# Performance work log

Measured on AMD Instinct MI355X. Metric: run time of the kernel, lower is better.

The kernel has to match this reference:

```python
import jax, jax.numpy as jnp
import numpy as np

WS = 8            # window size
OWIN = 12         # overlapping window: int(8*0.5)+8
HEADS = 4
DHEAD = 16
INNER = 64        # HEADS*DHEAD
DIM = 48
B, H, W = 4, 192, 192
HN, WN = H // WS, W // WS
NW = HN * WN
NK = NW // 2      # deterministic hard-token keep count (ratio=0.5, E[gumbel rate]=0.5)
SCALE = DHEAD ** -0.5


def conv1x1(x, w, b=None):
    y = jnp.einsum('bchw,oc->bohw', x, w)
    return y if b is None else y + b[:, None, None]


def win_part(x):
    # 'b c (h dh) (w dw) -> b (h w) (dh dw) c'
    b, c, h, w = x.shape
    x = x.reshape(b, c, h // WS, WS, w // WS, WS).transpose(0, 2, 4, 3, 5, 1)
    return x.reshape(b, (h // WS) * (w // WS), WS * WS, c)


def win_unpart(x, h, w):
    b, n, l, c = x.shape
    x = x.reshape(b, h // WS, w // WS, WS, WS, c).transpose(0, 5, 1, 3, 2, 4)
    return x.reshape(b, c, h, w)


def unfold_overlap(x):
    # nn.Unfold(kernel=OWIN, stride=WS, pad=(OWIN-WS)//2) -> (b, NW, OWIN^2, c)
    pad = (OWIN - WS) // 2
    xp = jnp.pad(x, ((0, 0), (0, 0), (pad, pad), (pad, pad)))
    hi = (jnp.arange(HN) * WS)[:, None] + jnp.arange(OWIN)[None]
    wi = (jnp.arange(WN) * WS)[:, None] + jnp.arange(OWIN)[None]
    p = xp[:, :, hi[:, None, :, None], wi[None, :, None, :]]  # (b,c,HN,WN,OWIN,OWIN)
    b, c = x.shape[:2]
    return p.reshape(b, c, NW, OWIN * OWIN).transpose(0, 2, 3, 1)


def rel_to_abs(x):
    b, l, m = x.shape
    r = (m + 1) // 2
    x = jnp.pad(x, ((0, 0), (0, 0), (0, 1)))
    flat = jnp.pad(x.reshape(b, l * (m + 1)), ((0, 0), (0, m - l)))
    return flat.reshape(b, l + 1, m)[:, :l, m - r:]


def relative_logits_1d(q, rel_k):
    b, h, w, d = q.shape
    r = (rel_k.shape[0] + 1) // 2
    logits = jnp.einsum('bxyd,rd->bxyr', q, rel_k)
    logits = rel_to_abs(logits.reshape(b * h, w, -1)).reshape(b, h, w, r)
    return jnp.broadcast_to(logits[:, :, None, :, :], (b, h, r, w, r))


def rel_pos_emb(q, rel_h, rel_w):
    # q: (B_, WS*WS, d) -> (B_, WS*WS, OWIN*OWIN)
    B_, L, d = q.shape
    q4 = q.reshape(B_, WS, WS, d)
    lw = relative_logits_1d(q4, rel_w).transpose(0, 1, 3, 2, 4).reshape(B_, L, -1)
    lh = relative_logits_1d(q4.transpose(0, 2, 1, 3), rel_h).transpose(0, 3, 1, 4, 2).reshape(B_, L, -1)
    return lw + lh


def reference(x, condition_global, wq, bq, wk, bk, wv, bv, w_in, b_in, ln_w, ln_b,
              w_sa, b_sa, w_m1, b_m1, w_m2, b_m2, rel_h, rel_w, w_out, b_out):
    b = x.shape[0]
    qs = conv1x1(x, wq, bq)
    ks = conv1x1(x, wk, bk)
    vs = conv1x1(x, wv, bv)

    # deformable condition: per-window normalized coordinate grid
    lin = jnp.linspace(-1.0, 1.0, WS, dtype=x.dtype)
    gy, gx = jnp.meshgrid(lin, lin, indexing='ij')
    wind = jnp.tile(jnp.stack([gy, gx]), (1, HN, WN))
    cond = jnp.concatenate([vs, condition_global, jnp.broadcast_to(wind, (b, 2, H, W))], axis=1)

    # PredictorLG (inference routing)
    t = conv1x1(cond, w_in, b_in)
    mu = t.mean(1, keepdims=True)
    var = ((t - mu) ** 2).mean(1, keepdims=True)
    t = (t - mu) / jnp.sqrt(var + 1e-6)
    t = t * ln_w[:, None, None] + ln_b[:, None, None]
    t = jax.nn.leaky_relu(t, 0.1)
    sa = jax.nn.sigmoid(jax.lax.conv_general_dilated(
        t, w_sa, (1, 1), ((1, 1), (1, 1)),
        dimension_numbers=('NCHW', 'OIHW', 'NCHW')) + b_sa[:, None, None])
    m = win_part(t.mean(1, keepdims=True)).reshape(b, NW, WS * WS)
    h1 = jax.nn.leaky_relu(m @ w_m1.T + b_m1, 0.1)
    pred = jax.nn.softmax(h1 @ w_m2.T + b_m2, axis=-1)
    score = pred[:, :, 0]
    order = jnp.argsort(-score, axis=1)
    idx1, idx2 = order[:, :NK], order[:, NK:]

    # hard branch: gather -> overlapping window attention with rel-pos bias
    qw = jnp.take_along_axis(win_part(qs), idx1[:, :, None, None], axis=1)       # (b,NK,WS^2,INNER)
    kw = jnp.take_along_axis(unfold_overlap(ks), idx1[:, :, None, None], axis=1)  # (b,NK,OWIN^2,INNER)
    vw = jnp.take_along_axis(unfold_overlap(vs), idx1[:, :, None, None], axis=1)
    qh = qw.reshape(b, NK, WS * WS, HEADS, DHEAD)
    kh = kw.reshape(b, NK, OWIN * OWIN, HEADS, DHEAD)
    vh = vw.reshape(b, NK, OWIN * OWIN, HEADS, DHEAD)
    sim = SCALE * jnp.einsum('bnqhd,bnkhd->bnhqk', qh, kh)
    rp = rel_pos_emb(qh.transpose(0, 1, 3, 2, 4).reshape(b * NK * HEADS, WS * WS, DHEAD), rel_h, rel_w)
    sim = sim + rp.reshape(b, NK, HEADS, WS * WS, OWIN * OWIN)
    attn = jax.nn.softmax(sim, axis=-1)
    hard = jnp.einsum('bnhqk,bnkhd->bnqhd', attn, vh).reshape(b, NK, WS * WS, INNER)

    # easy branch: spatial-attention-gated values
    easy = jnp.take_along_axis(win_part(vs * sa), idx2[:, :, None, None], axis=1)

    # scatter-merge (batch_index_fill)
    bar = jnp.arange(b)[:, None]
    merged = jnp.zeros((b, NW, WS * WS, INNER), x.dtype)
    merged = merged.at[bar, idx1].set(hard).at[bar, idx2].set(easy)
    out = win_unpart(merged, H, W)
    return conv1x1(out, w_out, b_out)


def setup_inputs() -> dict:
    key = jax.random.key(0)
    k = jax.random.split(key, 16)
    rn = lambda kk, s, sc=0.05: jax.random.normal(kk, s, jnp.float32) * sc
    return {
        'x': jax.random.normal(k[0], (B, DIM, H, W), jnp.float32),
        'condition_global': jax.random.normal(k[1], (B, 2, H, W), jnp.float32),
        'wq': rn(k[2], (INNER, DIM)), 'bq': jnp.zeros((INNER,), jnp.float32),
        'wk': rn(k[3], (INNER, DIM)), 'bk': jnp.zeros((INNER,), jnp.float32),
        'wv': rn(k[4], (INNER, DIM)), 'bv': jnp.zeros((INNER,), jnp.float32),
        'w_in': rn(k[5], (17, 68)), 'b_in': jnp.zeros((17,), jnp.float32),
        'ln_w': jnp.ones((17,), jnp.float32), 'ln_b': jnp.zeros((17,), jnp.float32),
        'w_sa': rn(k[6], (1, 17, 3, 3)), 'b_sa': jnp.zeros((1,), jnp.float32),
        'w_m1': rn(k[7], (WS, WS * WS)), 'b_m1': jnp.zeros((WS,), jnp.float32),
        'w_m2': rn(k[8], (2, WS)), 'b_m2': jnp.zeros((2,), jnp.float32),
        'rel_h': rn(k[9], (2 * OWIN - 1, DHEAD), DHEAD ** -0.5),
        'rel_w': rn(k[10], (2 * OWIN - 1, DHEAD), DHEAD ** -0.5),
        'w_out': rn(k[11], (DIM, INNER)), 'b_out': jnp.zeros((DIM,), jnp.float32),
    }
```

## Files before the change

kernel.cpp:

```cpp
#include <hip/hip_runtime.h>
#include <math.h>

#define Hh 192
#define Ww 192
#define HWc 36864
#define Bc 4
#define NWc 576
#define NKc 288
#define WNc 24

typedef _Float16 h2_t __attribute__((ext_vector_type(2)));
typedef _Float16 f16x4 __attribute__((ext_vector_type(4)));
typedef float f32x4 __attribute__((ext_vector_type(4)));
typedef unsigned u32x2 __attribute__((ext_vector_type(2)));
__device__ __forceinline__ h2_t u2h(unsigned u) { return __builtin_bit_cast(h2_t, u); }
__device__ __forceinline__ unsigned h2u(h2_t h) { return __builtin_bit_cast(unsigned, h); }
__device__ __forceinline__ h2_t pkrtz(float a, float b) {
    return __builtin_bit_cast(h2_t, __builtin_amdgcn_cvt_pkrtz(a, b));
}
__device__ __forceinline__ f16x4 pk4(float4 v) {
    u32x2 p = { h2u(pkrtz(v.x, v.y)), h2u(pkrtz(v.z, v.w)) };
    return __builtin_bit_cast(f16x4, p);
}
#define L2E 1.44269504f

__global__ __launch_bounds__(256, 1) void k_qkv(const float* __restrict__ x,
    const float* __restrict__ wq, const float* __restrict__ bq,
    const float* __restrict__ wk, const float* __restrict__ bk,
    const float* __restrict__ wvw, const float* __restrict__ bv,
    _Float16* __restrict__ q, _Float16* __restrict__ k, float* __restrict__ v)
{
    __shared__ float xs[132][52];

    int tid = threadIdx.x;
    int blk = blockIdx.x;
    int b = blk / 288;
    int g0 = (blk % 288) * 128;
    const float* xb = x + (size_t)b * 48 * HWc + g0;

    #pragma unroll
    for (int it = 0; it < 24; ++it) {
        int i = it * 256 + tid;
        int c = i >> 7, px = i & 127;
        xs[px][c] = xb[(size_t)c * HWc + px];
    }

    int ln = tid & 63, wave = tid >> 6;
    int dgrp = ln >> 4;
    __syncthreads();

    size_t pbase = (size_t)b * HWc + g0;

    {
        f16x4 Aq[4][3], Ak[4][3];
        #pragma unroll
        for (int ot = 0; ot < 4; ++ot)
            #pragma unroll
            for (int ks = 0; ks < 3; ++ks) {
                int oc = ot * 16 + (ln & 15);
                Aq[ot][ks] = pk4(*(const float4*)(wq + oc * 48 + ks * 16 + dgrp * 4));
                Ak[ot][ks] = pk4(*(const float4*)(wk + oc * 48 + ks * 16 + dgrp * 4));
            }
        float4 bqf[4], bkf[4];
        #pragma unroll
        for (int ot = 0; ot < 4; ++ot) {
            bqf[ot] = *(const float4*)(bq + ot * 16 + dgrp * 4);
            bkf[ot] = *(const float4*)(bk + ot * 16 + dgrp * 4);
        }

        #pragma unroll
        for (int t2 = 0; t2 < 2; ++t2) {
            int tn = wave * 2 + t2;
            int px = tn * 16 + (ln & 15);
            f16x4 Bf[3];
            #pragma unroll
            for (int ks = 0; ks < 3; ++ks)
                Bf[ks] = pk4(*(const float4*)&xs[px][ks * 16 + dgrp * 4]);

            #pragma unroll
            for (int ot = 0; ot < 4; ++ot) {
                f32x4 Dq = { bqf[ot].x, bqf[ot].y, bqf[ot].z, bqf[ot].w };
                f32x4 Dk = { bkf[ot].x, bkf[ot].y, bkf[ot].z, bkf[ot].w };
                #pragma unroll
                for (int ks = 0; ks < 3; ++ks) {
                    Dq = __builtin_amdgcn_mfma_f32_16x16x16f16(Aq[ot][ks], Bf[ks], Dq, 0, 0, 0);
                    Dk = __builtin_amdgcn_mfma_f32_16x16x16f16(Ak[ot][ks], Bf[ks], Dk, 0, 0, 0);
                }
                u32x2 q2 = { h2u(pkrtz(Dq[0], Dq[1])), h2u(pkrtz(Dq[2], Dq[3])) };
                u32x2 k2 = { h2u(pkrtz(Dk[0], Dk[1])), h2u(pkrtz(Dk[2], Dk[3])) };
                size_t off = (pbase + (size_t)px) * 64 + ot * 16 + dgrp * 4;
                *(u32x2*)(q + off) = q2;
                *(u32x2*)(k + off) = k2;
            }
        }
    }

    {
        float4 Wv[12];
        #pragma unroll
        for (int j = 0; j < 12; ++j) Wv[j] = *(const float4*)(wvw + ln * 48 + j * 4);
        float bvv = bv[ln];

        int p0 = wave * 32;
        #pragma unroll 1
        for (int g4 = 0; g4 < 8; ++g4) {
            int px = p0 + g4 * 4;
            float a0 = bvv, a1 = bvv, a2 = bvv, a3 = bvv;
            #pragma unroll
            for (int j = 0; j < 12; ++j) {
                float4 x0 = *(const float4*)&xs[px + 0][j * 4];
                float4 x1 = *(const float4*)&xs[px + 1][j * 4];
                float4 x2 = *(const float4*)&xs[px + 2][j * 4];
                float4 x3 = *(const float4*)&xs[px + 3][j * 4];
                a0 = fmaf(x0.x, Wv[j].x, a0); a0 = fmaf(x0.y, Wv[j].y, a0);
                a0 = fmaf(x0.z, Wv[j].z, a0); a0 = fmaf(x0.w, Wv[j].w, a0);
                a1 = fmaf(x1.x, Wv[j].x, a1); a1 = fmaf(x1.y, Wv[j].y, a1);
                a1 = fmaf(x1.z, Wv[j].z, a1); a1 = fmaf(x1.w, Wv[j].w, a1);
                a2 = fmaf(x2.x, Wv[j].x, a2); a2 = fmaf(x2.y, Wv[j].y, a2);
                a2 = fmaf(x2.z, Wv[j].z, a2); a2 = fmaf(x2.w, Wv[j].w, a2);
                a3 = fmaf(x3.x, Wv[j].x, a3); a3 = fmaf(x3.y, Wv[j].y, a3);
                a3 = fmaf(x3.z, Wv[j].z, a3); a3 = fmaf(x3.w, Wv[j].w, a3);
            }
            v[(pbase + (size_t)(px + 0)) * 64 + ln] = a0;
            v[(pbase + (size_t)(px + 1)) * 64 + ln] = a1;
            v[(pbase + (size_t)(px + 2)) * 64 + ln] = a2;
            v[(pbase + (size_t)(px + 3)) * 64 + ln] = a3;
        }
    }
}

__global__ __launch_bounds__(192) void k_condsa(const float* __restrict__ vs,
    const float* __restrict__ cg,
    const float* __restrict__ w_in, const float* __restrict__ b_in,
    const float* __restrict__ ln_w, const float* __restrict__ ln_b,
    const float* __restrict__ w_sa, const float* __restrict__ b_sa,
    float* __restrict__ sa, float* __restrict__ mpix)
{
    __shared__ float tl[3][17][194];

    int px = threadIdx.x;
    int blk = blockIdx.x;
    int b = blk / Hh;
    int y = blk % Hh;
    const float step = 2.0f / 7.0f;
    float gx_in = -1.0f + step * (float)(px & 7);

    #pragma unroll 1
    for (int r = 0; r < 3; ++r) {
        int yy = y - 1 + r;
        if ((unsigned)yy >= 192u) continue;
        size_t prem = (size_t)yy * Ww + px;

        float in[68];
        const float* vp = vs + ((size_t)b * HWc + prem) * 64;
        #pragma unroll
        for (int c = 0; c < 64; c += 4) {
            float4 t4 = *(const float4*)(vp + c);
            in[c] = t4.x; in[c+1] = t4.y; in[c+2] = t4.z; in[c+3] = t4.w;
        }
        in[64] = cg[((size_t)b * 2 + 0) * HWc + prem];
        in[65] = cg[((size_t)b * 2 + 1) * HWc + prem];
        in[66] = -1.0f + step * (float)(yy & 7);
        in[67] = gx_in;

        float tv[17];
        float mu = 0.f;
        #pragma unroll
        for (int o = 0; o < 17; ++o) {
            float a = b_in[o];
            const float* wr = w_in + o * 68;
            #pragma unroll
            for (int c = 0; c < 68; ++c) a = fmaf(in[c], wr[c], a);
            tv[o] = a;
            mu += a;
        }
        mu *= (1.f / 17.f);
        float var = 0.f;
        #pragma unroll
        for (int o = 0; o < 17; ++o) { float d = tv[o] - mu; var = fmaf(d, d, var); }
        var *= (1.f / 17.f);
        float rstd = 1.f / sqrtf(var + 1e-6f);

        float msum = 0.f;
        #pragma unroll
        for (int o = 0; o < 17; ++o) {
            float z = (tv[o] - mu) * rstd * ln_w[o] + ln_b[o];
            z = (z >= 0.f) ? z : 0.1f * z;
            tl[r][o][px] = z;
            msum += z;
        }
        if (r == 1) mpix[(size_t)b * HWc + prem] = msum * (1.f / 17.f);
    }
    __syncthreads();

    float a = b_sa[0];
    #pragma unroll 1
    for (int c = 0; c < 17; ++c) {
        const float* wr = w_sa + c * 9;
        #pragma unroll
        for (int ki = 0; ki < 3; ++ki) {
            int yy = y + ki - 1;
            if ((unsigned)yy >= 192u) continue;
            #pragma unroll
            for (int kj = 0; kj < 3; ++kj) {
                int xc = px + kj - 1;
                if ((unsigned)xc >= 192u) continue;
                a = fmaf(tl[ki][c][xc], wr[ki * 3 + kj], a);
            }
        }
    }
    sa[(size_t)b * HWc + (size_t)y * Ww + px] = 1.f / (1.f + expf(-a));
}

__global__ __launch_bounds__(576) void k_score(const float* __restrict__ mpix,
    const float* __restrict__ w_m1, const float* __restrict__ b_m1,
    const float* __restrict__ w_m2, const float* __restrict__ b_m2,
    int* __restrict__ hardl, int* __restrict__ easyl)
{
    __shared__ float sc[NWc];
    int b = blockIdx.x;
    int w = threadIdx.x;
    {
        int hy = w / WNc, wx = w % WNc;
        const float* mp = mpix + (size_t)b * HWc + (hy * 8) * Ww + wx * 8;
        float m[64];
        #pragma unroll
        for (int l = 0; l < 64; ++l) m[l] = mp[(l >> 3) * Ww + (l & 7)];
        float h1[8];
        #pragma unroll
        for (int j = 0; j < 8; ++j) {
            float a = b_m1[j];
            const float* wr = w_m1 + j * 64;
            #pragma unroll
            for (int l = 0; l < 64; ++l) a = fmaf(m[l], wr[l], a);
            h1[j] = (a >= 0.f) ? a : 0.1f * a;
        }
        float l0 = b_m2[0], l1 = b_m2[1];
        #pragma unroll
        for (int j = 0; j < 8; ++j) {
            l0 = fmaf(h1[j], w_m2[j], l0);
            l1 = fmaf(h1[j], w_m2[8 + j], l1);
        }
        float mx = fmaxf(l0, l1);
        float e0 = expf(l0 - mx), e1 = expf(l1 - mx);
        sc[w] = e0 / (e0 + e1);
    }
    __syncthreads();
    float s = sc[w];
    int cnt = 0;
    for (int w2 = 0; w2 < NWc; ++w2) {
        float s2 = sc[w2];
        cnt += ((s2 > s) || (s2 == s && w2 < w)) ? 1 : 0;
    }
    if (cnt < NKc) hardl[b * NKc + cnt] = w;
    else           easyl[b * NKc + (cnt - NKc)] = w;
}

__global__ __launch_bounds__(256) void k_hard(const _Float16* __restrict__ qs,
    const _Float16* __restrict__ ks, const float* __restrict__ vsb,
    const int* __restrict__ hardl,
    const float* __restrict__ relh, const float* __restrict__ relw,
    const float* __restrict__ w_out, const float* __restrict__ b_out,
    float* __restrict__ out)
{
    __shared__ __align__(16) unsigned char smem[53760];
    unsigned char* Kl  = smem;
    unsigned char* Vt  = smem + 18432;
    unsigned char* Rel = smem + 37376;
    _Float16 (*mldsh)[72] = (_Float16 (*)[72])smem;

    int tid = threadIdx.x;
    int blk = blockIdx.x;
    int b = blk / NKc;
    int n = hardl[blk];
    int hy = n / WNc, wx = n % WNc;
    int y0 = hy * 8, x0 = wx * 8;

    #pragma unroll
    for (int i = 0; i < 9; ++i) {
        int idx = i * 256 + tid;
        int px = idx >> 4, c4 = idx & 15;
        int py = px / 12, pxx = px - py * 12;
        int ky = y0 - 2 + py, kx = x0 - 2 + pxx;
        bool ok = ((unsigned)ky < 192u) && ((unsigned)kx < 192u);
        int kyc = min(max(ky, 0), 191), kxc = min(max(kx, 0), 191);
        size_t poff = ((size_t)(b * HWc) + kyc * Ww + kxc) * 64 + c4 * 4;
        uint2 k2 = *(const uint2*)(ks + poff);
        float4 v4 = *(const float4*)(vsb + poff);
        if (!ok) { k2 = make_uint2(0, 0); v4 = make_float4(0, 0, 0, 0); }
        int hd = c4 >> 2, d0 = (c4 & 3) * 4;
        *(uint2*)(Kl + hd * 4608 + px * 32 + (c4 & 3) * 8) = k2;
        _Float16* vh = (_Float16*)(Vt + hd * 4736);
        vh[(d0 + 0) * 148 + px] = (_Float16)v4.x;
        vh[(d0 + 1) * 148 + px] = (_Float16)v4.y;
        vh[(d0 + 2) * 148 + px] = (_Float16)v4.z;
        vh[(d0 + 3) * 148 + px] = (_Float16)v4.w;
    }

    int h = __builtin_amdgcn_readfirstlane(tid >> 6);
    int l = tid & 63;
    int dgrp = l >> 4;

    {
        int qr = l >> 3, qc = l & 7;
        const _Float16* qp = qs + ((size_t)(b * HWc) + (y0 + qr) * Ww + (x0 + qc)) * 64 + h * 16;
        uint4 q0 = *(const uint4*)qp;
        uint4 q1 = *(const uint4*)(qp + 8);
        h2_t qhp[8] = { u2h(q0.x), u2h(q0.y), u2h(q0.z), u2h(q0.w),
                        u2h(q1.x), u2h(q1.y), u2h(q1.z), u2h(q1.w) };
        float qv[16];
        #pragma unroll
        for (int j = 0; j < 8; ++j) { qv[2*j] = (float)qhp[j].x; qv[2*j+1] = (float)qhp[j].y; }

        float rw[12], rh[12];
        #pragma unroll
        for (int kc = 0; kc < 12; ++kc) {
            const float* rp = relw + (kc - qc + 11) * 16;
            float a = 0.f;
            #pragma unroll
            for (int j = 0; j < 4; ++j) {
                float4 t4 = *(const float4*)(rp + j * 4);
                a = fmaf(qv[j*4+0], t4.x, a); a = fmaf(qv[j*4+1], t4.y, a);
                a = fmaf(qv[j*4+2], t4.z, a); a = fmaf(qv[j*4+3], t4.w, a);
            }
            rw[kc] = a;
        }
        #pragma unroll
        for (int kr = 0; kr < 12; ++kr) {
            const float* rp = relh + (kr - qr + 11) * 16;
            float a = 0.f;
            #pragma unroll
            for (int j = 0; j < 4; ++j) {
                float4 t4 = *(const float4*)(rp + j * 4);
                a = fmaf(qv[j*4+0], t4.x, a); a = fmaf(qv[j*4+1], t4.y, a);
                a = fmaf(qv[j*4+2], t4.z, a); a = fmaf(qv[j*4+3], t4.w, a);
            }
            rh[kr] = a;
        }
        unsigned rr[16];
        #pragma unroll
        for (int j = 0; j < 6; ++j) rr[j]     = h2u(pkrtz(L2E * rw[2*j], L2E * rw[2*j+1]));
        #pragma unroll
        for (int j = 0; j < 6; ++j) rr[6 + j] = h2u(pkrtz(L2E * rh[2*j], L2E * rh[2*j+1]));
        rr[12] = rr[13] = rr[14] = rr[15] = 0u;
        uint4* dst = (uint4*)(Rel + h * 4096 + l * 64);
        dst[0] = make_uint4(rr[0], rr[1], rr[2],  rr[3]);
        dst[1] = make_uint4(rr[4], rr[5], rr[6],  rr[7]);
        dst[2] = make_uint4(rr[8], rr[9], rr[10], rr[11]);
        dst[3] = make_uint4(rr[12], rr[13], rr[14], rr[15]);
    }
    __syncthreads();

    f16x4 qb[4], rb1[4], rb2[4];
    {
        const h2_t qsc = { (_Float16)(0.25f * L2E), (_Float16)(0.25f * L2E) };
        #pragma unroll
        for (int tn = 0; tn < 4; ++tn) {
            int q = tn * 16 + (l & 15);
            int qr = q >> 3, qc = q & 7;
            uint2 raw = *(const uint2*)(qs + ((size_t)(b * HWc) + (y0 + qr) * Ww + (x0 + qc)) * 64 + h * 16 + dgrp * 4);
            h2_t lo = u2h(raw.x) * qsc, hi = u2h(raw.y) * qsc;
            u32x2 packed = { h2u(lo), h2u(hi) };
            qb[tn] = __builtin_bit_cast(f16x4, packed);
            const unsigned char* rbase = Rel + h * 4096 + q * 64 + dgrp * 8;
            rb1[tn] = *(const f16x4*)rbase;
            rb2[tn] = *(const f16x4*)(rbase + 32);
        }
    }

    f32x4 Oacc[4];
    float lsum[4];
    #pragma unroll
    for (int tn = 0; tn < 4; ++tn) { Oacc[tn] = (f32x4){0.f,0.f,0.f,0.f}; lsum[tn] = 0.f; }
    const f32x4 zf = {0.f, 0.f, 0.f, 0.f};
    const float SH = 3.0f * L2E;

    f16x4 kaA = *(const f16x4*)(Kl + h * 4608 + (l & 15) * 32 + dgrp * 8);
    f16x4 vaA = *(const f16x4*)(Vt + h * 4736 + (l & 15) * 296 + (dgrp * 4) * 2);

    #pragma unroll 1
    for (int tm = 0; tm < 9; ++tm) {
        int tmn = (tm + 1 < 9) ? tm + 1 : 0;
        f16x4 kaB = *(const f16x4*)(Kl + h * 4608 + (tmn * 16 + (l & 15)) * 32 + dgrp * 8);
        f16x4 vaB = *(const f16x4*)(Vt + h * 4736 + (l & 15) * 296 + (tmn * 16 + dgrp * 4) * 2);

        int key = tm * 16 + (l & 15);
        int kr = (key * 2731) >> 15;
        int kc = key - kr * 12;
        f16x4 oh1, oh2;
        #pragma unroll
        for (int i = 0; i < 4; ++i) {
            int a1 = 4 * dgrp + i;
            bool v1 = (a1 < 12) ? (kc == a1) : (kr == a1 - 12);
            oh1[i] = v1 ? (_Float16)1.0f : (_Float16)0.0f;
            int a2 = 16 + 4 * dgrp + i;
            bool v2 = (a2 < 24) && (kr == a2 - 12);
            oh2[i] = v2 ? (_Float16)1.0f : (_Float16)0.0f;
        }

        #pragma unroll
        for (int tn = 0; tn < 4; ++tn) {
            f32x4 s = __builtin_amdgcn_mfma_f32_16x16x16f16(kaA, qb[tn],  zf, 0, 0, 0);
            s       = __builtin_amdgcn_mfma_f32_16x16x16f16(oh1, rb1[tn], s,  0, 0, 0);
            s       = __builtin_amdgcn_mfma_f32_16x16x16f16(oh2, rb2[tn], s,  0, 0, 0);
            float e0 = exp2f(s[0] - SH);
            float e1 = exp2f(s[1] - SH);
            float e2 = exp2f(s[2] - SH);
            float e3 = exp2f(s[3] - SH);
            lsum[tn] += (e0 + e1) + (e2 + e3);
            u32x2 pp = { h2u(pkrtz(e0, e1)), h2u(pkrtz(e2, e3)) };
            f16x4 pb = __builtin_bit_cast(f16x4, pp);
            Oacc[tn] = __builtin_amdgcn_mfma_f32_16x16x16f16(vaA, pb, Oacc[tn], 0, 0, 0);
        }
        kaA = kaB; vaA = vaB;
    }

    __syncthreads();
    #pragma unroll
    for (int tn = 0; tn < 4; ++tn) {
        float s = lsum[tn];
        s += __shfl_xor(s, 16);
        s += __shfl_xor(s, 32);
        float inv = 1.f / s;
        int q = tn * 16 + (l & 15);
        u32x2 w2 = { h2u(pkrtz(Oacc[tn][0] * inv, Oacc[tn][1] * inv)),
                     h2u(pkrtz(Oacc[tn][2] * inv, Oacc[tn][3] * inv)) };
        *(u32x2*)&mldsh[q][h * 16 + dgrp * 4] = w2;
    }
    __syncthreads();

    {
        int tn2 = h;
        int pxl = tn2 * 16 + (l & 15);
        f16x4 bf[4];
        #pragma unroll
        for (int ks = 0; ks < 4; ++ks)
            bf[ks] = *(const f16x4*)&mldsh[pxl][ks * 16 + dgrp * 4];

        int gy = y0 + (pxl >> 3), gx = x0 + (pxl & 7);
        #pragma unroll
        for (int ot = 0; ot < 3; ++ot) {
            float4 bi = *(const float4*)(b_out + ot * 16 + dgrp * 4);
            f32x4 Cacc = { bi.x, bi.y, bi.z, bi.w };
            #pragma unroll
            for (int ks = 0; ks < 4; ++ks) {
                float4 wv = *(const float4*)(w_out + (ot * 16 + (l & 15)) * 64 + ks * 16 + dgrp * 4);
                Cacc = __builtin_amdgcn_mfma_f32_16x16x16f16(pk4(wv), bf[ks], Cacc, 0, 0, 0);
            }
            #pragma unroll
            for (int i = 0; i < 4; ++i)
                out[((size_t)(b * 48 + ot * 16 + dgrp * 4 + i)) * HWc + gy * Ww + gx] = Cacc[i];
        }
    }
}

__global__ __launch_bounds__(256) void k_easy(const float* __restrict__ vsb,
    const float* __restrict__ sab, const int* __restrict__ easyl,
    const float* __restrict__ w_out, const float* __restrict__ b_out,
    float* __restrict__ out)
{
    __shared__ __align__(16) _Float16 mldsh[64][72];

    int tid = threadIdx.x;
    int blk = blockIdx.x;
    int b = blk / NKc;
    int n = easyl[blk];
    int hy = n / WNc, wx = n % WNc;
    int y0 = hy * 8, x0 = wx * 8;

    {
        int l = tid >> 2, part = tid & 3;
        int gy = y0 + (l >> 3), gx = x0 + (l & 7);
        const float* vp = vsb + ((size_t)(b * HWc) + gy * Ww + gx) * 64 + part * 16;
        float sv = sab[(size_t)b * HWc + gy * Ww + gx];
        #pragma unroll
        for (int j = 0; j < 4; ++j) {
            float4 v4 = *(const float4*)(vp + j * 4);
            u32x2 w2 = { h2u(pkrtz(v4.x * sv, v4.y * sv)),
                         h2u(pkrtz(v4.z * sv, v4.w * sv)) };
            *(u32x2*)&mldsh[l][part * 16 + j * 4] = w2;
        }
    }
    __syncthreads();

    {
        int l = tid & 63;
        int tn2 = __builtin_amdgcn_readfirstlane(tid >> 6);
        int dgrp = l >> 4;
        int pxl = tn2 * 16 + (l & 15);
        f16x4 bf[4];
        #pragma unroll
        for (int ks = 0; ks < 4; ++ks)
            bf[ks] = *(const f16x4*)&mldsh[pxl][ks * 16 + dgrp * 4];

        int gy = y0 + (pxl >> 3), gx = x0 + (pxl & 7);
        #pragma unroll
        for (int ot = 0; ot < 3; ++ot) {
            float4 bi = *(const float4*)(b_out + ot * 16 + dgrp * 4);
            f32x4 Cacc = { bi.x, bi.y, bi.z, bi.w };
            #pragma unroll
            for (int ks = 0; ks < 4; ++ks) {
                float4 wv = *(const float4*)(w_out + (ot * 16 + (l & 15)) * 64 + ks * 16 + dgrp * 4);
                Cacc = __builtin_amdgcn_mfma_f32_16x16x16f16(pk4(wv), bf[ks], Cacc, 0, 0, 0);
            }
            #pragma unroll
            for (int i = 0; i < 4; ++i)
                out[((size_t)(b * 48 + ot * 16 + dgrp * 4 + i)) * HWc + gy * Ww + gx] = Cacc[i];
        }
    }
}

extern "C" void kernel_launch(void* const* d_in, const int* in_sizes, int n_in,
                              void* d_out, int out_size, void* d_ws, size_t ws_size,
                              hipStream_t stream)
{
    const float* x    = (const float*)d_in[0];
    const float* cg   = (const float*)d_in[1];
    const float* wq   = (const float*)d_in[2];
    const float* bq   = (const float*)d_in[3];
    const float* wk   = (const float*)d_in[4];
    const float* bk   = (const float*)d_in[5];
    const float* wv   = (const float*)d_in[6];
    const float* bv   = (const float*)d_in[7];
    const float* w_in = (const float*)d_in[8];
    const float* b_in = (const float*)d_in[9];
    const float* ln_w = (const float*)d_in[10];
    const float* ln_b = (const float*)d_in[11];
    const float* w_sa = (const float*)d_in[12];
    const float* b_sa = (const float*)d_in[13];
    const float* w_m1 = (const float*)d_in[14];
    const float* b_m1 = (const float*)d_in[15];
    const float* w_m2 = (const float*)d_in[16];
    const float* b_m2 = (const float*)d_in[17];
    const float* rel_h= (const float*)d_in[18];
    const float* rel_w= (const float*)d_in[19];
    const float* w_out= (const float*)d_in[20];
    const float* b_out= (const float*)d_in[21];
    float* out = (float*)d_out;

    _Float16* qsh = (_Float16*)d_ws;
    _Float16* ksh = qsh + (size_t)Bc * 64 * HWc;
    float* vs   = (float*)(ksh + (size_t)Bc * 64 * HWc);
    float* sa   = vs + (size_t)Bc * 64 * HWc;
    float* mpix = sa + (size_t)Bc * HWc;
    int*   hardl= (int*)(mpix + (size_t)Bc * HWc);
    int*   easyl= hardl + Bc * NKc;

    k_qkv   <<<1152, 256, 0, stream>>>(x, wq, bq, wk, bk, wv, bv, qsh, ksh, vs);
    k_condsa<<<Bc * Hh, 192, 0, stream>>>(vs, cg, w_in, b_in, ln_w, ln_b, w_sa, b_sa, sa, mpix);
    k_score <<<4, 576, 0, stream>>>(mpix, w_m1, b_m1, w_m2, b_m2, hardl, easyl);
    k_easy  <<<1152, 256, 0, stream>>>(vs, sa, easyl, w_out, b_out, out);
    k_hard  <<<1152, 256, 0, stream>>>(qsh, ksh, vs, hardl, rel_h, rel_w, w_out, b_out, out);
}
```

Baseline: 193.5 us.

## Compute V projection with split-fp16 MFMA and compact relative-logit LDS table

```diff
diff --git a/kernel.cpp b/kernel.cpp
--- a/kernel.cpp
+++ b/kernel.cpp
@@ -96,35 +96,49 @@
     }
 
     {
-        float4 Wv[12];
-        #pragma unroll
-        for (int j = 0; j < 12; ++j) Wv[j] = *(const float4*)(wvw + ln * 48 + j * 4);
-        float bvv = bv[ln];
-
-        int p0 = wave * 32;
-        #pragma unroll 1
-        for (int g4 = 0; g4 < 8; ++g4) {
-            int px = p0 + g4 * 4;
-            float a0 = bvv, a1 = bvv, a2 = bvv, a3 = bvv;
-            #pragma unroll
-            for (int j = 0; j < 12; ++j) {
-                float4 x0 = *(const float4*)&xs[px + 0][j * 4];
-                float4 x1 = *(const float4*)&xs[px + 1][j * 4];
-                float4 x2 = *(const float4*)&xs[px + 2][j * 4];
-                float4 x3 = *(const float4*)&xs[px + 3][j * 4];
-                a0 = fmaf(x0.x, Wv[j].x, a0); a0 = fmaf(x0.y, Wv[j].y, a0);
-                a0 = fmaf(x0.z, Wv[j].z, a0); a0 = fmaf(x0.w, Wv[j].w, a0);
-                a1 = fmaf(x1.x, Wv[j].x, a1); a1 = fmaf(x1.y, Wv[j].y, a1);
-                a1 = fmaf(x1.z, Wv[j].z, a1); a1 = fmaf(x1.w, Wv[j].w, a1);
-                a2 = fmaf(x2.x, Wv[j].x, a2); a2 = fmaf(x2.y, Wv[j].y, a2);
-                a2 = fmaf(x2.z, Wv[j].z, a2); a2 = fmaf(x2.w, Wv[j].w, a2);
-                a3 = fmaf(x3.x, Wv[j].x, a3); a3 = fmaf(x3.y, Wv[j].y, a3);
-                a3 = fmaf(x3.z, Wv[j].z, a3); a3 = fmaf(x3.w, Wv[j].w, a3);
-            }
-            v[(pbase + (size_t)(px + 0)) * 64 + ln] = a0;
-            v[(pbase + (size_t)(px + 1)) * 64 + ln] = a1;
-            v[(pbase + (size_t)(px + 2)) * 64 + ln] = a2;
-            v[(pbase + (size_t)(px + 3)) * 64 + ln] = a3;
+        f16x4 Avh[4][3], Avl[4][3];
+        #pragma unroll
+        for (int ot = 0; ot < 4; ++ot)
+            #pragma unroll
+            for (int ks = 0; ks < 3; ++ks) {
+                int oc = ot * 16 + (ln & 15);
+                float4 w4 = *(const float4*)(wvw + oc * 48 + ks * 16 + dgrp * 4);
+                f16x4 wh = pk4(w4);
+                float4 wr = make_float4(w4.x - (float)wh[0], w4.y - (float)wh[1],
+                                        w4.z - (float)wh[2], w4.w - (float)wh[3]);
+                Avh[ot][ks] = wh;
+                Avl[ot][ks] = pk4(wr);
+            }
+        float4 bvf[4];
+        #pragma unroll
+        for (int ot = 0; ot < 4; ++ot) bvf[ot] = *(const float4*)(bv + ot * 16 + dgrp * 4);
+
+        #pragma unroll
+        for (int t2 = 0; t2 < 2; ++t2) {
+            int tn = wave * 2 + t2;
+            int px = tn * 16 + (ln & 15);
+            f16x4 Bh[3], Bl[3];
+            #pragma unroll
+            for (int ks = 0; ks < 3; ++ks) {
+                float4 x4 = *(const float4*)&xs[px][ks * 16 + dgrp * 4];
+                f16x4 xh = pk4(x4);
+                float4 xr = make_float4(x4.x - (float)xh[0], x4.y - (float)xh[1],
+                                        x4.z - (float)xh[2], x4.w - (float)xh[3]);
+                Bh[ks] = xh;
+                Bl[ks] = pk4(xr);
+            }
+            #pragma unroll
+            for (int ot = 0; ot < 4; ++ot) {
+                f32x4 D = { bvf[ot].x, bvf[ot].y, bvf[ot].z, bvf[ot].w };
+                #pragma unroll
+                for (int ks = 0; ks < 3; ++ks) {
+                    D = __builtin_amdgcn_mfma_f32_16x16x16f16(Avh[ot][ks], Bh[ks], D, 0, 0, 0);
+                    D = __builtin_amdgcn_mfma_f32_16x16x16f16(Avh[ot][ks], Bl[ks], D, 0, 0, 0);
+                    D = __builtin_amdgcn_mfma_f32_16x16x16f16(Avl[ot][ks], Bh[ks], D, 0, 0, 0);
+                }
+                *(float4*)(v + (pbase + (size_t)px) * 64 + ot * 16 + dgrp * 4) =
+                    make_float4(D[0], D[1], D[2], D[3]);
+            }
         }
     }
 }
@@ -263,7 +277,7 @@
     const float* __restrict__ w_out, const float* __restrict__ b_out,
     float* __restrict__ out)
 {
-    __shared__ __align__(16) unsigned char smem[53760];
+    __shared__ __align__(16) unsigned char smem[49728];
     unsigned char* Kl  = smem;
     unsigned char* Vt  = smem + 18432;
     unsigned char* Rel = smem + 37376;
@@ -296,6 +310,7 @@
         vh[(d0 + 2) * 148 + px] = (_Float16)v4.z;
         vh[(d0 + 3) * 148 + px] = (_Float16)v4.w;
     }
+    if (tid < 16) *(unsigned*)(Rel + 12288 + tid * 4) = 0u;
 
     int h = __builtin_amdgcn_readfirstlane(tid >> 6);
     int l = tid & 63;
@@ -337,17 +352,15 @@
             }
             rh[kr] = a;
         }
-        unsigned rr[16];
+        unsigned rr[12];
         #pragma unroll
         for (int j = 0; j < 6; ++j) rr[j]     = h2u(pkrtz(L2E * rw[2*j], L2E * rw[2*j+1]));
         #pragma unroll
         for (int j = 0; j < 6; ++j) rr[6 + j] = h2u(pkrtz(L2E * rh[2*j], L2E * rh[2*j+1]));
-        rr[12] = rr[13] = rr[14] = rr[15] = 0u;
-        uint4* dst = (uint4*)(Rel + h * 4096 + l * 64);
+        uint4* dst = (uint4*)(Rel + h * 3072 + l * 48);
         dst[0] = make_uint4(rr[0], rr[1], rr[2],  rr[3]);
         dst[1] = make_uint4(rr[4], rr[5], rr[6],  rr[7]);
         dst[2] = make_uint4(rr[8], rr[9], rr[10], rr[11]);
-        dst[3] = make_uint4(rr[12], rr[13], rr[14], rr[15]);
     }
     __syncthreads();
 
@@ -362,7 +375,7 @@
             h2_t lo = u2h(raw.x) * qsc, hi = u2h(raw.y) * qsc;
             u32x2 packed = { h2u(lo), h2u(hi) };
             qb[tn] = __builtin_bit_cast(f16x4, packed);
-            const unsigned char* rbase = Rel + h * 4096 + q * 64 + dgrp * 8;
+            const unsigned char* rbase = Rel + h * 3072 + q * 48 + dgrp * 8;
             rb1[tn] = *(const f16x4*)rbase;
             rb2[tn] = *(const f16x4*)(rbase + 32);
         }
```

After: 190.2 us. No clear change (-1.7%).
